# Kernel optimization log

Hardware: AMD Instinct MI355X
Metric: run time of the kernel (lower is better)

Reference implementation:

```python
import jax, jax.numpy as jnp
import numpy as np

N = 100000      # nodes
E = 1200000     # edges
H = 64          # hidden_channels
L = 8           # num_layers
G = 100         # graphs in batch
ALPHA = 0.1
THETA = 0.5
EPS = 1e-5      # BatchNorm1d eps


def setup_inputs() -> dict:
    key = jax.random.key(0)
    ks = jax.random.split(key, 12)
    s = 0.05
    pos = jax.random.normal(ks[0], (N, 3), dtype=jnp.float32)
    edge_index = jax.random.randint(ks[1], (2, E), 0, N, dtype=jnp.int32)
    batch = jnp.sort(jax.random.randint(ks[2], (N,), 0, G, dtype=jnp.int32))
    return {
        "pos": pos,
        "edge_index": edge_index,
        "batch": batch,
        "lin0_w": jax.random.normal(ks[3], (3, H), dtype=jnp.float32) * s,
        "lin0_b": jnp.zeros((H,), jnp.float32),
        "conv_w": jax.random.normal(ks[4], (L, H, H), dtype=jnp.float32) * s,
        "lin1_w": jax.random.normal(ks[5], (H, H), dtype=jnp.float32) * s,
        "lin1_b": jnp.zeros((H,), jnp.float32),
        "mlp1_w": jax.random.normal(ks[6], (H, H), dtype=jnp.float32) * s,
        "mlp1_b": jnp.zeros((H,), jnp.float32),
        "bn1_g": jnp.ones((H,), jnp.float32),
        "bn1_b": jnp.zeros((H,), jnp.float32),
        "mlp2_w": jax.random.normal(ks[7], (H, H), dtype=jnp.float32) * s,
        "mlp2_b": jnp.zeros((H,), jnp.float32),
        "bn2_g": jnp.ones((H,), jnp.float32),
        "bn2_b": jnp.zeros((H,), jnp.float32),
        "out_w": jax.random.normal(ks[8], (H, 10), dtype=jnp.float32) * s,
        "out_b": jnp.zeros((10,), jnp.float32),
    }


def _bn(z, g, b):
    # BatchNorm1d, training-mode batch statistics
    mu = z.mean(axis=0)
    var = z.var(axis=0)
    return g * (z - mu) * jax.lax.rsqrt(var + EPS) + b


def reference(pos, edge_index, batch, lin0_w, lin0_b, conv_w, lin1_w, lin1_b,
              mlp1_w, mlp1_b, bn1_g, bn1_b, mlp2_w, mlp2_b, bn2_g, bn2_b,
              out_w, out_b):
    src, dst = edge_index[0], edge_index[1]
    x = jax.nn.relu(pos @ lin0_w + lin0_b)   # [N, H]
    x0 = x
    for l in range(L):
        beta = float(np.log(THETA / (l + 1) + 1.0))
        # GCN2Conv (normalize=False, shared_weights=True):
        # sum-aggregate neighbors, initial residual, identity mapping
        agg = jax.ops.segment_sum(x[src], dst, num_segments=N)   # [N, H]
        h = (1.0 - ALPHA) * agg + ALPHA * x0
        x = jax.nn.relu((1.0 - beta) * h + beta * (h @ conv_w[l]))
    x = x @ lin1_w + lin1_b
    pooled = jax.ops.segment_max(x, batch, num_segments=G)       # [G, H]
    pooled = jnp.where(jnp.isfinite(pooled), pooled, 0.0)        # guard empty segments
    h1 = jax.nn.relu(_bn(pooled @ mlp1_w + mlp1_b, bn1_g, bn1_b))
    h2 = jax.nn.relu(_bn(h1 @ mlp2_w + mlp2_b, bn2_g, bn2_b))
    logits = h2 @ out_w + out_b                                  # [G, 10]
    return jax.nn.log_softmax(logits, axis=-1)
```

## Files before the change

kernel.cpp:

```cpp
#include <hip/hip_runtime.h>
#include <math.h>

#define NNODES 100000
#define NEDGES 1200000
#define HD 64
#define NLAYERS 8
#define NGRAPH 100
#define PPART 32

__global__ void lin0_k(const float* __restrict__ pos, const float* __restrict__ w,
                       const float* __restrict__ b, float* __restrict__ x0, int total) {
    int i = blockIdx.x * blockDim.x + threadIdx.x;
    if (i >= total) return;
    int n = i >> 6, h = i & 63;
    float p0 = pos[n * 3 + 0], p1 = pos[n * 3 + 1], p2 = pos[n * 3 + 2];
    float v = fmaf(p0, w[h], fmaf(p1, w[64 + h], fmaf(p2, w[128 + h], b[h])));
    x0[i] = fmaxf(v, 0.0f);
}

__global__ void hist_k(const int* __restrict__ dst, int* __restrict__ deg,
                       int* __restrict__ rank, int E) {
    int e = blockIdx.x * blockDim.x + threadIdx.x;
    if (e < E) rank[e] = atomicAdd(&deg[dst[e]], 1);
}

__global__ void scan_part_k(const int* __restrict__ deg, int* __restrict__ bsum, int n) {
    __shared__ int s[256];
    int t = threadIdx.x;
    int i = blockIdx.x * 256 + t;
    s[t] = (i < n) ? deg[i] : 0;
    __syncthreads();
    for (int off = 128; off > 0; off >>= 1) {
        if (t < off) s[t] += s[t + off];
        __syncthreads();
    }
    if (t == 0) bsum[blockIdx.x] = s[0];
}

__global__ void scan_mid_k(const int* __restrict__ bsum, int* __restrict__ boff,
                           int nblk, int* __restrict__ roff, int n) {
    __shared__ int s[512];
    int t = threadIdx.x;
    int v = (t < nblk) ? bsum[t] : 0;
    s[t] = v;
    __syncthreads();
    for (int off = 1; off < 512; off <<= 1) {
        int u = (t >= off) ? s[t - off] : 0;
        __syncthreads();
        s[t] += u;
        __syncthreads();
    }
    if (t < nblk) boff[t] = s[t] - v;
    if (t == nblk - 1) roff[n] = s[t];
}

__global__ void scan_final_k(const int* __restrict__ deg, const int* __restrict__ boff,
                             int* __restrict__ roff, int n) {
    __shared__ int s[256];
    int t = threadIdx.x;
    int i = blockIdx.x * 256 + t;
    int v = (i < n) ? deg[i] : 0;
    s[t] = v;
    __syncthreads();
    for (int off = 1; off < 256; off <<= 1) {
        int u = (t >= off) ? s[t - off] : 0;
        __syncthreads();
        s[t] += u;
        __syncthreads();
    }
    if (i < n) roff[i] = boff[blockIdx.x] + s[t] - v;
}

__global__ void fill_k(const int* __restrict__ src, const int* __restrict__ dst,
                       const int* __restrict__ roff, const int* __restrict__ rank,
                       int* __restrict__ csr, int E) {
    int e = blockIdx.x * blockDim.x + threadIdx.x;
    if (e < E) csr[roff[dst[e]] + rank[e]] = src[e];
}

__global__ __launch_bounds__(256, 8) void layer_k(
    const float* __restrict__ xin, float* __restrict__ xout,
    const float* __restrict__ x0, const float* __restrict__ W,
    const int* __restrict__ roff, const int* __restrict__ csr,
    float beta, int total_waves) {
    __shared__ __align__(16) float MT[64 * 64];
    __shared__ __align__(16) float hrow[4][64];
    const int tid   = threadIdx.x;
    const int lane  = tid & 63;
    const int wslot = tid >> 6;
    const float omb = 1.0f - beta;
    for (int idx = tid; idx < 4096; idx += 256) {
        int k = idx >> 6, j = idx & 63;
        float m = beta * W[idx];
        if (k == j) m += omb;
        MT[j * 64 + (((k >> 2) ^ (j & 15)) << 2) + (k & 3)] = m;
    }
    __syncthreads();
    const int wid0 = (blockIdx.x * blockDim.x + tid) >> 6;
    for (int n = wid0; n < NNODES; n += total_waves) {
        const int beg = roff[n], end = roff[n + 1];
        float x0v = x0[(n << 6) + lane];
        float s0 = 0.0f, s1 = 0.0f, s2 = 0.0f, s3 = 0.0f;
        int i = beg;
        for (; i + 8 <= end; i += 8) {
            int e0 = csr[i + 0], e1 = csr[i + 1], e2 = csr[i + 2], e3 = csr[i + 3];
            int e4 = csr[i + 4], e5 = csr[i + 5], e6 = csr[i + 6], e7 = csr[i + 7];
            float a0 = xin[(e0 << 6) + lane];
            float a1 = xin[(e1 << 6) + lane];
            float a2 = xin[(e2 << 6) + lane];
            float a3 = xin[(e3 << 6) + lane];
            float a4 = xin[(e4 << 6) + lane];
            float a5 = xin[(e5 << 6) + lane];
            float a6 = xin[(e6 << 6) + lane];
            float a7 = xin[(e7 << 6) + lane];
            s0 += a0; s1 += a1; s2 += a2; s3 += a3;
            s0 += a4; s1 += a5; s2 += a6; s3 += a7;
        }
        for (; i + 4 <= end; i += 4) {
            int e0 = csr[i + 0], e1 = csr[i + 1], e2 = csr[i + 2], e3 = csr[i + 3];
            s0 += xin[(e0 << 6) + lane];
            s1 += xin[(e1 << 6) + lane];
            s2 += xin[(e2 << 6) + lane];
            s3 += xin[(e3 << 6) + lane];
        }
        for (; i < end; ++i) s0 += xin[(csr[i] << 6) + lane];
        float agg = (s0 + s1) + (s2 + s3);
        float h = fmaf(0.9f, agg, 0.1f * x0v);
        hrow[wslot][lane] = h;
        __builtin_amdgcn_wave_barrier();
        float a0 = 0.0f, a1 = 0.0f, a2 = 0.0f, a3 = 0.0f;
#pragma unroll
        for (int g = 0; g < 16; ++g) {
            float4 hv = *(const float4*)&hrow[wslot][g * 4];
            float4 mv = *(const float4*)&MT[(lane << 6) + ((g ^ (lane & 15)) << 2)];
            a0 = fmaf(hv.x, mv.x, a0);
            a1 = fmaf(hv.y, mv.y, a1);
            a2 = fmaf(hv.z, mv.z, a2);
            a3 = fmaf(hv.w, mv.w, a3);
        }
        __builtin_amdgcn_wave_barrier();
        float o = (a0 + a1) + (a2 + a3);
        xout[(n << 6) + lane] = fmaxf(o, 0.0f);
    }
}

__device__ __forceinline__ int lbound(const int* __restrict__ a, int n, int v) {
    int lo = 0, hi = n;
    while (lo < hi) { int mid = (lo + hi) >> 1; if (a[mid] < v) lo = mid + 1; else hi = mid; }
    return lo;
}

__global__ __launch_bounds__(256, 8) void poolpart_k(
    const float* __restrict__ xin, const float* __restrict__ W,
    const float* __restrict__ bvec, const int* __restrict__ batch,
    float* __restrict__ pmax) {
    __shared__ __align__(16) float MT[64 * 64];
    __shared__ __align__(16) float hrow[4][64];
    __shared__ float wm[4][64];
    const int tid   = threadIdx.x;
    const int lane  = tid & 63;
    const int wslot = tid >> 6;
    for (int idx = tid; idx < 4096; idx += 256) {
        int k = idx >> 6, j = idx & 63;
        MT[j * 64 + (((k >> 2) ^ (j & 15)) << 2) + (k & 3)] = W[idx];
    }
    __syncthreads();
    const int g = blockIdx.x / PPART, part = blockIdx.x % PPART;
    const int lo = lbound(batch, NNODES, g);
    const int hi = lbound(batch, NNODES, g + 1);
    const int cnt = hi - lo;
    const int qlo = lo + (cnt * part) / PPART;
    const int qhi = lo + (cnt * (part + 1)) / PPART;
    const float bias = bvec[lane];
    float vmax = -INFINITY;
    for (int n = qlo + wslot; n < qhi; n += 4) {
        hrow[wslot][lane] = xin[(n << 6) + lane];
        __builtin_amdgcn_wave_barrier();
        float a0 = bias, a1 = 0.0f, a2 = 0.0f, a3 = 0.0f;
#pragma unroll
        for (int gg = 0; gg < 16; ++gg) {
            float4 hv = *(const float4*)&hrow[wslot][gg * 4];
            float4 mv = *(const float4*)&MT[(lane << 6) + ((gg ^ (lane & 15)) << 2)];
            a0 = fmaf(hv.x, mv.x, a0);
            a1 = fmaf(hv.y, mv.y, a1);
            a2 = fmaf(hv.z, mv.z, a2);
            a3 = fmaf(hv.w, mv.w, a3);
        }
        __builtin_amdgcn_wave_barrier();
        vmax = fmaxf(vmax, (a0 + a1) + (a2 + a3));
    }
    wm[wslot][lane] = vmax;
    __syncthreads();
    if (tid < 64) {
        float m = fmaxf(fmaxf(wm[0][tid], wm[1][tid]), fmaxf(wm[2][tid], wm[3][tid]));
        pmax[blockIdx.x * 64 + tid] = m;
    }
}

__global__ void poolcomb_k(const float* __restrict__ pmax, float* __restrict__ pooled) {
    int i = blockIdx.x * blockDim.x + threadIdx.x;
    if (i >= NGRAPH * 64) return;
    int g = i >> 6, lane = i & 63;
    float m = -INFINITY;
    for (int p = 0; p < PPART; ++p)
        m = fmaxf(m, pmax[(PPART * g + p) * 64 + lane]);
    pooled[i] = m;
}

__global__ __launch_bounds__(256) void head_k(
    const float* __restrict__ pooled,
    const float* __restrict__ m1w, const float* __restrict__ m1b,
    const float* __restrict__ g1, const float* __restrict__ be1,
    const float* __restrict__ m2w, const float* __restrict__ m2b,
    const float* __restrict__ g2, const float* __restrict__ be2,
    const float* __restrict__ ow, const float* __restrict__ ob,
    float* __restrict__ out) {
    __shared__ float A[NGRAPH * 64];
    __shared__ float B[NGRAPH * 64];
    __shared__ float mu[64], rs[64];
    __shared__ float LG[NGRAPH * 10];
    int t = threadIdx.x;
    for (int i = t; i < NGRAPH * 64; i += 256) {
        float f = pooled[i];
        if (!isfinite(f)) f = 0.0f;
        A[i] = f;
    }
    __syncthreads();
    for (int i = t; i < NGRAPH * 64; i += 256) {
        int g = i >> 6, j = i & 63;
        float acc = m1b[j];
        for (int k = 0; k < 64; ++k) acc = fmaf(A[(g << 6) + k], m1w[k * 64 + j], acc);
        B[i] = acc;
    }
    __syncthreads();
    if (t < 64) {
        float sm = 0.0f, sq = 0.0f;
        for (int g = 0; g < NGRAPH; ++g) { float z = B[g * 64 + t]; sm += z; sq += z * z; }
        float m = sm * (1.0f / NGRAPH);
        float var = sq * (1.0f / NGRAPH) - m * m;
        mu[t] = m; rs[t] = rsqrtf(var + 1e-5f);
    }
    __syncthreads();
    for (int i = t; i < NGRAPH * 64; i += 256) {
        int j = i & 63;
        float z = fmaf((B[i] - mu[j]) * rs[j], g1[j], be1[j]);
        A[i] = fmaxf(z, 0.0f);
    }
    __syncthreads();
    for (int i = t; i < NGRAPH * 64; i += 256) {
        int g = i >> 6, j = i & 63;
        float acc = m2b[j];
        for (int k = 0; k < 64; ++k) acc = fmaf(A[(g << 6) + k], m2w[k * 64 + j], acc);
        B[i] = acc;
    }
    __syncthreads();
    if (t < 64) {
        float sm = 0.0f, sq = 0.0f;
        for (int g = 0; g < NGRAPH; ++g) { float z = B[g * 64 + t]; sm += z; sq += z * z; }
        float m = sm * (1.0f / NGRAPH);
        float var = sq * (1.0f / NGRAPH) - m * m;
        mu[t] = m; rs[t] = rsqrtf(var + 1e-5f);
    }
    __syncthreads();
    for (int i = t; i < NGRAPH * 64; i += 256) {
        int j = i & 63;
        float z = fmaf((B[i] - mu[j]) * rs[j], g2[j], be2[j]);
        A[i] = fmaxf(z, 0.0f);
    }
    __syncthreads();
    for (int i = t; i < NGRAPH * 10; i += 256) {
        int g = i / 10, j = i - g * 10;
        float acc = ob[j];
        for (int k = 0; k < 64; ++k) acc = fmaf(A[(g << 6) + k], ow[k * 10 + j], acc);
        LG[i] = acc;
    }
    __syncthreads();
    if (t < NGRAPH) {
        float m = -1e30f;
        for (int j = 0; j < 10; ++j) m = fmaxf(m, LG[t * 10 + j]);
        float s = 0.0f;
        for (int j = 0; j < 10; ++j) s += expf(LG[t * 10 + j] - m);
        float lse = m + logf(s);
        for (int j = 0; j < 10; ++j) out[t * 10 + j] = LG[t * 10 + j] - lse;
    }
}

extern "C" void kernel_launch(void* const* d_in, const int* in_sizes, int n_in,
                              void* d_out, int out_size, void* d_ws, size_t ws_size,
                              hipStream_t stream) {
    const float* pos   = (const float*)d_in[0];
    const int*   eidx  = (const int*)d_in[1];
    const int*   batch = (const int*)d_in[2];
    const float* l0w   = (const float*)d_in[3];
    const float* l0b   = (const float*)d_in[4];
    const float* cw    = (const float*)d_in[5];
    const float* l1w   = (const float*)d_in[6];
    const float* l1b   = (const float*)d_in[7];
    const float* m1w   = (const float*)d_in[8];
    const float* m1b   = (const float*)d_in[9];
    const float* g1    = (const float*)d_in[10];
    const float* b1    = (const float*)d_in[11];
    const float* m2w   = (const float*)d_in[12];
    const float* m2b   = (const float*)d_in[13];
    const float* g2    = (const float*)d_in[14];
    const float* b2    = (const float*)d_in[15];
    const float* ow    = (const float*)d_in[16];
    const float* ob    = (const float*)d_in[17];
    float* out = (float*)d_out;
    const int* src = eidx;
    const int* dst = eidx + NEDGES;

    size_t off = 0;
    auto alloc = [&](size_t bytes) -> void* {
        void* p = (char*)d_ws + off;
        off += (bytes + 255) & ~(size_t)255;
        return p;
    };
    float*    x0     = (float*)alloc((size_t)NNODES * 64 * 4);
    float*    xA     = (float*)alloc((size_t)NNODES * 64 * 4);
    float*    xB     = (float*)alloc((size_t)NNODES * 64 * 4);
    int*      deg    = (int*)alloc((size_t)NNODES * 4);
    int*      roff   = (int*)alloc((size_t)(NNODES + 1) * 4);
    const int NBLK   = (NNODES + 255) / 256;
    int*      bsum   = (int*)alloc((size_t)NBLK * 4);
    int*      boff   = (int*)alloc((size_t)NBLK * 4);
    int*      csr    = (int*)alloc((size_t)NEDGES * 4);
    float*    pooled = (float*)alloc((size_t)NGRAPH * 64 * 4);
    float*    pmax   = (float*)alloc((size_t)NGRAPH * PPART * 64 * 4);
    int*      rank   = (int*)xB;

    hipMemsetAsync(deg, 0, (size_t)NNODES * 4, stream);
    {
        int total = NNODES * 64;
        lin0_k<<<(total + 255) / 256, 256, 0, stream>>>(pos, l0w, l0b, x0, total);
    }
    hist_k<<<(NEDGES + 255) / 256, 256, 0, stream>>>(dst, deg, rank, NEDGES);
    scan_part_k<<<NBLK, 256, 0, stream>>>(deg, bsum, NNODES);
    scan_mid_k<<<1, 512, 0, stream>>>(bsum, boff, NBLK, roff, NNODES);
    scan_final_k<<<NBLK, 256, 0, stream>>>(deg, boff, roff, NNODES);
    fill_k<<<(NEDGES + 255) / 256, 256, 0, stream>>>(src, dst, roff, rank, csr, NEDGES);

    const int LBLOCKS = 2048;
    const int TW = LBLOCKS * 256 / 64;
    const float* cur = x0;
    for (int l = 0; l < NLAYERS; ++l) {
        float beta = (float)log(0.5 / (double)(l + 1) + 1.0);
        float* nxt = (l & 1) ? xB : xA;
        layer_k<<<LBLOCKS, 256, 0, stream>>>(cur, nxt, x0, cw + (size_t)l * 4096,
                                             roff, csr, beta, TW);
        cur = nxt;
    }
    poolpart_k<<<NGRAPH * PPART, 256, 0, stream>>>(cur, l1w, l1b, batch, pmax);
    poolcomb_k<<<(NGRAPH * 64 + 255) / 256, 256, 0, stream>>>(pmax, pooled);
    head_k<<<1, 256, 0, stream>>>(pooled, m1w, m1b, g1, b1, m2w, m2b, g2, b2, ow, ob, out);
}
```

Before: 650.7 us.

## Store layer activations in fp16 with per-layer power-of-two rescaling

Node feature buffers between GCN2 layers are stored as fp16 instead of fp32, halving the bytes moved by the neighbor gather, which dominates layer time. To keep values in fp16 range, each layer scales its weight matrix by 1/8 and the x0 residual by a matching power of two, and the pooling kernel multiplies the result by 2^24 before adding the bias. ReLU commutes with positive scaling, so the intended output is unchanged apart from fp16 rounding, which may add error.

```diff
diff --git a/kernel.cpp b/kernel.cpp
--- a/kernel.cpp
+++ b/kernel.cpp
@@ -1,4 +1,5 @@
 #include <hip/hip_runtime.h>
+#include <hip/hip_fp16.h>
 #include <math.h>
 
 #define NNODES 100000
@@ -7,15 +8,22 @@
 #define NLAYERS 8
 #define NGRAPH 100
 #define PPART 32
+#define C8 16777216.0f
+
+__device__ __forceinline__ float h2f(__half h) { return __half2float(h); }
+__device__ __forceinline__ __half f2h(float f) { return __float2half(f); }
 
 __global__ void lin0_k(const float* __restrict__ pos, const float* __restrict__ w,
-                       const float* __restrict__ b, float* __restrict__ x0, int total) {
+                       const float* __restrict__ b, float* __restrict__ x0f,
+                       __half* __restrict__ x0h, int total) {
     int i = blockIdx.x * blockDim.x + threadIdx.x;
     if (i >= total) return;
     int n = i >> 6, h = i & 63;
     float p0 = pos[n * 3 + 0], p1 = pos[n * 3 + 1], p2 = pos[n * 3 + 2];
     float v = fmaf(p0, w[h], fmaf(p1, w[64 + h], fmaf(p2, w[128 + h], b[h])));
-    x0[i] = fmaxf(v, 0.0f);
+    v = fmaxf(v, 0.0f);
+    x0f[i] = v;
+    x0h[i] = f2h(v);
 }
 
 __global__ void hist_k(const int* __restrict__ dst, int* __restrict__ deg,
@@ -79,10 +87,10 @@
 }
 
 __global__ __launch_bounds__(256, 8) void layer_k(
-    const float* __restrict__ xin, float* __restrict__ xout,
+    const __half* __restrict__ xin, __half* __restrict__ xout,
     const float* __restrict__ x0, const float* __restrict__ W,
     const int* __restrict__ roff, const int* __restrict__ csr,
-    float beta, int total_waves) {
+    float beta, float x0scale, int total_waves) {
     __shared__ __align__(16) float MT[64 * 64];
     __shared__ __align__(16) float hrow[4][64];
     const int tid   = threadIdx.x;
@@ -93,6 +101,7 @@
         int k = idx >> 6, j = idx & 63;
         float m = beta * W[idx];
         if (k == j) m += omb;
+        m *= 0.125f;
         MT[j * 64 + (((k >> 2) ^ (j & 15)) << 2) + (k & 3)] = m;
     }
     __syncthreads();
@@ -105,27 +114,27 @@
         for (; i + 8 <= end; i += 8) {
             int e0 = csr[i + 0], e1 = csr[i + 1], e2 = csr[i + 2], e3 = csr[i + 3];
             int e4 = csr[i + 4], e5 = csr[i + 5], e6 = csr[i + 6], e7 = csr[i + 7];
-            float a0 = xin[(e0 << 6) + lane];
-            float a1 = xin[(e1 << 6) + lane];
-            float a2 = xin[(e2 << 6) + lane];
-            float a3 = xin[(e3 << 6) + lane];
-            float a4 = xin[(e4 << 6) + lane];
-            float a5 = xin[(e5 << 6) + lane];
-            float a6 = xin[(e6 << 6) + lane];
-            float a7 = xin[(e7 << 6) + lane];
-            s0 += a0; s1 += a1; s2 += a2; s3 += a3;
-            s0 += a4; s1 += a5; s2 += a6; s3 += a7;
+            __half a0 = xin[(e0 << 6) + lane];
+            __half a1 = xin[(e1 << 6) + lane];
+            __half a2 = xin[(e2 << 6) + lane];
+            __half a3 = xin[(e3 << 6) + lane];
+            __half a4 = xin[(e4 << 6) + lane];
+            __half a5 = xin[(e5 << 6) + lane];
+            __half a6 = xin[(e6 << 6) + lane];
+            __half a7 = xin[(e7 << 6) + lane];
+            s0 += h2f(a0); s1 += h2f(a1); s2 += h2f(a2); s3 += h2f(a3);
+            s0 += h2f(a4); s1 += h2f(a5); s2 += h2f(a6); s3 += h2f(a7);
         }
         for (; i + 4 <= end; i += 4) {
             int e0 = csr[i + 0], e1 = csr[i + 1], e2 = csr[i + 2], e3 = csr[i + 3];
-            s0 += xin[(e0 << 6) + lane];
-            s1 += xin[(e1 << 6) + lane];
-            s2 += xin[(e2 << 6) + lane];
-            s3 += xin[(e3 << 6) + lane];
+            s0 += h2f(xin[(e0 << 6) + lane]);
+            s1 += h2f(xin[(e1 << 6) + lane]);
+            s2 += h2f(xin[(e2 << 6) + lane]);
+            s3 += h2f(xin[(e3 << 6) + lane]);
         }
-        for (; i < end; ++i) s0 += xin[(csr[i] << 6) + lane];
+        for (; i < end; ++i) s0 += h2f(xin[(csr[i] << 6) + lane]);
         float agg = (s0 + s1) + (s2 + s3);
-        float h = fmaf(0.9f, agg, 0.1f * x0v);
+        float h = fmaf(0.9f, agg, x0scale * x0v);
         hrow[wslot][lane] = h;
         __builtin_amdgcn_wave_barrier();
         float a0 = 0.0f, a1 = 0.0f, a2 = 0.0f, a3 = 0.0f;
@@ -140,7 +149,7 @@
         }
         __builtin_amdgcn_wave_barrier();
         float o = (a0 + a1) + (a2 + a3);
-        xout[(n << 6) + lane] = fmaxf(o, 0.0f);
+        xout[(n << 6) + lane] = f2h(fmaxf(o, 0.0f));
     }
 }
 
@@ -151,7 +160,7 @@
 }
 
 __global__ __launch_bounds__(256, 8) void poolpart_k(
-    const float* __restrict__ xin, const float* __restrict__ W,
+    const __half* __restrict__ xin, const float* __restrict__ W,
     const float* __restrict__ bvec, const int* __restrict__ batch,
     float* __restrict__ pmax) {
     __shared__ __align__(16) float MT[64 * 64];
@@ -174,9 +183,9 @@
     const float bias = bvec[lane];
     float vmax = -INFINITY;
     for (int n = qlo + wslot; n < qhi; n += 4) {
-        hrow[wslot][lane] = xin[(n << 6) + lane];
+        hrow[wslot][lane] = h2f(xin[(n << 6) + lane]);
         __builtin_amdgcn_wave_barrier();
-        float a0 = bias, a1 = 0.0f, a2 = 0.0f, a3 = 0.0f;
+        float a0 = 0.0f, a1 = 0.0f, a2 = 0.0f, a3 = 0.0f;
 #pragma unroll
         for (int gg = 0; gg < 16; ++gg) {
             float4 hv = *(const float4*)&hrow[wslot][gg * 4];
@@ -187,7 +196,8 @@
             a3 = fmaf(hv.w, mv.w, a3);
         }
         __builtin_amdgcn_wave_barrier();
-        vmax = fmaxf(vmax, (a0 + a1) + (a2 + a3));
+        float acc = (a0 + a1) + (a2 + a3);
+        vmax = fmaxf(vmax, fmaf(C8, acc, bias));
     }
     wm[wslot][lane] = vmax;
     __syncthreads();
@@ -316,23 +326,24 @@
         off += (bytes + 255) & ~(size_t)255;
         return p;
     };
-    float*    x0     = (float*)alloc((size_t)NNODES * 64 * 4);
-    float*    xA     = (float*)alloc((size_t)NNODES * 64 * 4);
-    float*    xB     = (float*)alloc((size_t)NNODES * 64 * 4);
-    int*      deg    = (int*)alloc((size_t)NNODES * 4);
-    int*      roff   = (int*)alloc((size_t)(NNODES + 1) * 4);
-    const int NBLK   = (NNODES + 255) / 256;
-    int*      bsum   = (int*)alloc((size_t)NBLK * 4);
-    int*      boff   = (int*)alloc((size_t)NBLK * 4);
-    int*      csr    = (int*)alloc((size_t)NEDGES * 4);
-    float*    pooled = (float*)alloc((size_t)NGRAPH * 64 * 4);
-    float*    pmax   = (float*)alloc((size_t)NGRAPH * PPART * 64 * 4);
-    int*      rank   = (int*)xB;
+    float*  x0f    = (float*)alloc((size_t)NNODES * 64 * 4);
+    __half* x0h    = (__half*)alloc((size_t)NNODES * 64 * 2);
+    __half* xA     = (__half*)alloc((size_t)NNODES * 64 * 2);
+    __half* xB     = (__half*)alloc((size_t)NNODES * 64 * 2);
+    int*    deg    = (int*)alloc((size_t)NNODES * 4);
+    int*    roff   = (int*)alloc((size_t)(NNODES + 1) * 4);
+    const int NBLK = (NNODES + 255) / 256;
+    int*    bsum   = (int*)alloc((size_t)NBLK * 4);
+    int*    boff   = (int*)alloc((size_t)NBLK * 4);
+    int*    csr    = (int*)alloc((size_t)NEDGES * 4);
+    float*  pooled = (float*)alloc((size_t)NGRAPH * 64 * 4);
+    float*  pmax   = (float*)alloc((size_t)NGRAPH * PPART * 64 * 4);
+    int*    rank   = (int*)xB;
 
     hipMemsetAsync(deg, 0, (size_t)NNODES * 4, stream);
     {
         int total = NNODES * 64;
-        lin0_k<<<(total + 255) / 256, 256, 0, stream>>>(pos, l0w, l0b, x0, total);
+        lin0_k<<<(total + 255) / 256, 256, 0, stream>>>(pos, l0w, l0b, x0f, x0h, total);
     }
     hist_k<<<(NEDGES + 255) / 256, 256, 0, stream>>>(dst, deg, rank, NEDGES);
     scan_part_k<<<NBLK, 256, 0, stream>>>(deg, bsum, NNODES);
@@ -342,12 +353,13 @@
 
     const int LBLOCKS = 2048;
     const int TW = LBLOCKS * 256 / 64;
-    const float* cur = x0;
+    const __half* cur = x0h;
     for (int l = 0; l < NLAYERS; ++l) {
-        float beta = (float)log(0.5 / (double)(l + 1) + 1.0);
-        float* nxt = (l & 1) ? xB : xA;
-        layer_k<<<LBLOCKS, 256, 0, stream>>>(cur, nxt, x0, cw + (size_t)l * 4096,
-                                             roff, csr, beta, TW);
+        float beta    = (float)log(0.5 / (double)(l + 1) + 1.0);
+        float x0scale = (float)(0.1 * ldexp(1.0, -3 * l));
+        __half* nxt = (l & 1) ? xB : xA;
+        layer_k<<<LBLOCKS, 256, 0, stream>>>(cur, nxt, x0f, cw + (size_t)l * 4096,
+                                             roff, csr, beta, x0scale, TW);
         cur = nxt;
     }
     poolpart_k<<<NGRAPH * PPART, 256, 0, stream>>>(cur, l1w, l1b, batch, pmax);
```

Measured after the change: 620.9 us. 1.05x faster.
